# Optimization experiments

Hardware: AMD Instinct MI355X
Metric: run time of the kernel (lower is better)

The kernel has to match this reference:

```python
import jax, jax.numpy as jnp
import numpy as np

B, N, C = 2, 784, 384
D_STATE, D_CONV, EXPAND = 64, 4, 2
D_INNER = EXPAND * C           # 768
DT_RANK = -(-C // 16)          # 24
NB, BS = 4, C // 4             # EinFFT blocks
SCALE = 0.02


def setup_inputs() -> dict:
    key = jax.random.key(0)
    ks = jax.random.split(key, 16)
    rn = lambda k, s, sc=SCALE: jax.random.normal(k, s, jnp.float32) * sc
    A = jnp.tile(jnp.arange(1, D_STATE + 1, dtype=jnp.float32), (D_INNER, 1))
    return {
        'x': jax.random.normal(ks[0], (B, N, C), jnp.float32),
        'H': 28, 'W': 28,
        'ln1_w': jnp.ones((C,), jnp.float32), 'ln1_b': jnp.zeros((C,), jnp.float32),
        'in_proj_w': rn(ks[1], (2 * D_INNER, C)),
        'conv_w': rn(ks[2], (D_INNER, 1, D_CONV), 0.1),
        'conv_b': jnp.zeros((D_INNER,), jnp.float32),
        'x_proj_w': rn(ks[3], (DT_RANK + 2 * D_STATE, D_INNER)),
        'dt_proj_w': rn(ks[4], (D_INNER, DT_RANK), 0.1),
        'dt_proj_b': rn(ks[5], (D_INNER,), 0.1),
        'A_log': jnp.log(A),
        'Dp': jnp.ones((D_INNER,), jnp.float32),
        'out_proj_w': rn(ks[6], (C, D_INNER)),
        'ln2_w': jnp.ones((C,), jnp.float32), 'ln2_b': jnp.zeros((C,), jnp.float32),
        'cw1': rn(ks[7], (2, NB, BS, BS)), 'cb1': rn(ks[8], (2, NB, BS)),
        'cw2': rn(ks[9], (2, NB, BS, BS)), 'cb2': rn(ks[10], (2, NB, BS)),
    }


def _ln(x, w, b, eps=1e-5):
    mu = x.mean(-1, keepdims=True)
    var = ((x - mu) ** 2).mean(-1, keepdims=True)
    return (x - mu) * jax.lax.rsqrt(var + eps) * w + b


def _silu(x):
    return x * jax.nn.sigmoid(x)


def _mamba(x, in_proj_w, conv_w, conv_b, x_proj_w, dt_proj_w, dt_proj_b, A_log, Dp, out_proj_w):
    Bb, L, _ = x.shape
    di, ds = A_log.shape
    dt_rank = dt_proj_w.shape[1]
    xz = x @ in_proj_w.T                       # [B,L,2*di]
    xi, z = jnp.split(xz, 2, axis=-1)
    # causal depthwise conv1d (pad left d_conv-1)
    xc = jax.lax.conv_general_dilated(
        xi.transpose(0, 2, 1), conv_w, (1,), [(conv_w.shape[-1] - 1, 0)],
        feature_group_count=di, dimension_numbers=('NCH', 'OIH', 'NCH'))
    xc = _silu(xc + conv_b[None, :, None]).transpose(0, 2, 1)  # [B,L,di]
    dbl = xc @ x_proj_w.T
    dt, Bs, Cs = jnp.split(dbl, [dt_rank, dt_rank + ds], axis=-1)
    dt = jax.nn.softplus(dt @ dt_proj_w.T + dt_proj_b)          # [B,L,di]
    A = -jnp.exp(A_log)                                          # [di,ds]

    def step(h, inp):
        dt_t, B_t, C_t, u_t = inp                                # [B,di],[B,ds],[B,ds],[B,di]
        dA = jnp.exp(dt_t[:, :, None] * A)                       # [B,di,ds]
        h = h * dA + dt_t[:, :, None] * B_t[:, None, :] * u_t[:, :, None]
        y = jnp.einsum('bds,bs->bd', h, C_t)
        return h, y

    h0 = jnp.zeros((Bb, di, ds), x.dtype)
    xs = (dt.transpose(1, 0, 2), Bs.transpose(1, 0, 2), Cs.transpose(1, 0, 2), xc.transpose(1, 0, 2))
    _, ys = jax.lax.scan(step, h0, xs)                           # [L,B,di]
    y = ys.transpose(1, 0, 2) + xc * Dp
    y = y * _silu(z)
    return y @ out_proj_w.T


def _einfft(x, cw1, cb1, cw2, cb2, lam=0.01):
    Bb, Nn, Cc = x.shape
    nb, bs = cw1.shape[1], cw1.shape[2]
    xf = jnp.fft.fft2(x.reshape(Bb, Nn, nb, bs), axes=(1, 2), norm='ortho')
    mul = lambda t, w: jnp.einsum('...bd,bdk->...bk', t, w)
    r1 = jax.nn.relu(mul(xf.real, cw1[0]) - mul(xf.imag, cw1[1]) + cb1[0])
    i1 = jax.nn.relu(mul(xf.real, cw1[1]) + mul(xf.imag, cw1[0]) + cb1[1])
    r2 = mul(r1, cw2[0]) - mul(i1, cw2[1]) + cb2[0]
    i2 = mul(r1, cw2[1]) + mul(i1, cw2[0]) + cb2[1]
    shrink = lambda v: jnp.sign(v) * jnp.maximum(jnp.abs(v) - lam, 0.0)
    xcplx = shrink(r2) + 1j * shrink(i2)
    out = jnp.fft.ifft2(xcplx, axes=(1, 2), norm='ortho').real.astype(jnp.float32)
    return out.reshape(Bb, Nn, Cc)


def reference(x, H, W, ln1_w, ln1_b, in_proj_w, conv_w, conv_b, x_proj_w,
              dt_proj_w, dt_proj_b, A_log, Dp, out_proj_w, ln2_w, ln2_b,
              cw1, cb1, cw2, cb2):
    x = x + _mamba(_ln(x, ln1_w, ln1_b), in_proj_w, conv_w, conv_b, x_proj_w,
                   dt_proj_w, dt_proj_b, A_log, Dp, out_proj_w)
    x = x + _einfft(_ln(x, ln2_w, ln2_b), cw1, cb1, cw2, cb2)
    return x
```

## Files before the change

### kernel.cpp

```cpp
#include <hip/hip_runtime.h>
#include <math.h>

#define BB 2
#define NN 784
#define CC 384
#define DI 768
#define DS 64
#define DTR 24
#define ROWS (BB*NN)
#define NC 16
#define LC 49

typedef __attribute__((ext_vector_type(8))) short bf16x8;
typedef __attribute__((ext_vector_type(4))) float f32x4;

static __device__ inline short f2bf(float f){
  unsigned u = __float_as_uint(f);
  unsigned r = (u + 0x7fffu + ((u>>16)&1u)) >> 16;
  return (short)r;
}
static __device__ inline float bf2f(short v){
  return __uint_as_float(((unsigned)(unsigned short)v)<<16);
}
static __device__ inline float rdlane(float v, int t){
  return __uint_as_float(__builtin_amdgcn_readlane(__float_as_uint(v), t));
}
template<int CTRL>
static __device__ inline float qp_add(float x){
  int t = __builtin_amdgcn_update_dpp(0, __float_as_int(x), CTRL, 0xf, 0xf, false);
  return x + __int_as_float(t);
}
#define QP_XOR1 0xB1
#define QP_XOR2 0x4E

__global__ void k_zero4(float4* __restrict__ p, int n4){
  int i = blockIdx.x*256 + threadIdx.x;
  if (i < n4) p[i] = make_float4(0.f,0.f,0.f,0.f);
}

__global__ void k_ln(const float* __restrict__ x, const float* __restrict__ w,
                     const float* __restrict__ b, float* __restrict__ out, int rows){
  int row = blockIdx.x;
  if (row >= rows) return;
  int lane = threadIdx.x;
  const float* xr = x + (size_t)row*CC;
  float v[6]; float s = 0.f;
#pragma unroll
  for (int i=0;i<6;i++){ v[i] = xr[lane + 64*i]; s += v[i]; }
#pragma unroll
  for (int o=32;o;o>>=1) s += __shfl_xor(s,o);
  float mu = s * (1.f/CC);
  float vs = 0.f;
#pragma unroll
  for (int i=0;i<6;i++){ float d=v[i]-mu; vs += d*d; }
#pragma unroll
  for (int o=32;o;o>>=1) vs += __shfl_xor(vs,o);
  float rstd = rsqrtf(vs*(1.f/CC) + 1e-5f);
  float* orow = out + (size_t)row*CC;
#pragma unroll
  for (int i=0;i<6;i++){ int c = lane+64*i; orow[c] = (v[i]-mu)*rstd*w[c] + b[c]; }
}

__global__ void k_lnT(const float* __restrict__ x, const float* __restrict__ w,
                      const float* __restrict__ b, float* __restrict__ out){
  int row = blockIdx.x;
  if (row >= ROWS) return;
  int bb = row / NN, n = row % NN;
  int lane = threadIdx.x;
  const float* xr = x + (size_t)row*CC;
  float v[6]; float s = 0.f;
#pragma unroll
  for (int i=0;i<6;i++){ v[i] = xr[lane + 64*i]; s += v[i]; }
#pragma unroll
  for (int o=32;o;o>>=1) s += __shfl_xor(s,o);
  float mu = s * (1.f/CC);
  float vs = 0.f;
#pragma unroll
  for (int i=0;i<6;i++){ float d=v[i]-mu; vs += d*d; }
#pragma unroll
  for (int o=32;o;o>>=1) vs += __shfl_xor(vs,o);
  float rstd = rsqrtf(vs*(1.f/CC) + 1e-5f);
  float* ob = out + (size_t)bb*301056 + n;
#pragma unroll
  for (int i=0;i<6;i++){ int c = lane+64*i; ob[(size_t)c*NN] = (v[i]-mu)*rstd*w[c] + b[c]; }
}

template<int EPI, int ABF, int BBF, int SPLITK>
__global__ __launch_bounds__(256) void k_mgemm(
    const void* __restrict__ Ap, int lda, long long Azs,
    const void* __restrict__ Bp, int ldb, long long Bzs,
    const float* __restrict__ aux, int ldaux, long long auxzs,
    float* __restrict__ Y, int ldo, long long Ozs,
    int M, int N, int K, float alpha)
{
  __shared__ __align__(16) short As[64*32];
  __shared__ __align__(16) short Bs[64*32];
  int bz = blockIdx.z;
  int z  = bz / SPLITK, ks = bz % SPLITK;
  if (EPI == 1 || EPI == 2 || EPI == 3) aux += (size_t)z*auxzs;
  Y += (size_t)z*Ozs;
  int nk = (K + 31) >> 5;
  int per = (nk + SPLITK - 1) / SPLITK;
  int kbeg = ks*per*32;
  int kend = kbeg + per*32; if (kend > K) kend = K;
  int m0 = blockIdx.y*64, n0 = blockIdx.x*64;
  int t = threadIdx.x;
  int srow = t>>2, skg = t&3;
  int w = t>>6, lane = t&63;
  int wr = (w>>1)*32, wc = (w&1)*32;
  int l15 = lane&15, lh = lane>>4;
  f32x4 acc[2][2] = {};
  int sslot = skg ^ ((srow>>1)&3);
  for (int k0=kbeg; k0<kend; k0+=32){
    {
      int gm = m0 + srow, gk = k0 + skg*8;
      if (ABF){
        bf16x8 v = {};
        if (gm < M && gk < K) v = *(const bf16x8*)((const short*)Ap + (size_t)z*Azs + (size_t)gm*lda + gk);
        *(bf16x8*)(As + srow*32 + sslot*8) = v;
      } else {
        const float* Af = (const float*)Ap + (size_t)z*Azs;
        float4 v0 = {0,0,0,0}, v1 = {0,0,0,0};
        if (gm < M && gk < K){
          const float* p = Af + (size_t)gm*lda + gk;
          v0 = *(const float4*)p; v1 = *(const float4*)(p+4);
        }
        union { short s[8]; bf16x8 v; } pk;
        pk.s[0]=f2bf(v0.x); pk.s[1]=f2bf(v0.y); pk.s[2]=f2bf(v0.z); pk.s[3]=f2bf(v0.w);
        pk.s[4]=f2bf(v1.x); pk.s[5]=f2bf(v1.y); pk.s[6]=f2bf(v1.z); pk.s[7]=f2bf(v1.w);
        *(bf16x8*)(As + srow*32 + sslot*8) = pk.v;
      }
    }
    {
      int gn = n0 + srow, gk = k0 + skg*8;
      if (BBF){
        bf16x8 v = {};
        if (gn < N && gk < K) v = *(const bf16x8*)((const short*)Bp + (size_t)z*Bzs + (size_t)gn*ldb + gk);
        *(bf16x8*)(Bs + srow*32 + sslot*8) = v;
      } else {
        const float* Bf = (const float*)Bp + (size_t)z*Bzs;
        float4 v0 = {0,0,0,0}, v1 = {0,0,0,0};
        if (gn < N && gk < K){
          const float* p = Bf + (size_t)gn*ldb + gk;
          v0 = *(const float4*)p; v1 = *(const float4*)(p+4);
        }
        union { short s[8]; bf16x8 v; } pk;
        pk.s[0]=f2bf(v0.x); pk.s[1]=f2bf(v0.y); pk.s[2]=f2bf(v0.z); pk.s[3]=f2bf(v0.w);
        pk.s[4]=f2bf(v1.x); pk.s[5]=f2bf(v1.y); pk.s[6]=f2bf(v1.z); pk.s[7]=f2bf(v1.w);
        *(bf16x8*)(Bs + srow*32 + sslot*8) = pk.v;
      }
    }
    __syncthreads();
    bf16x8 af[2], bfr[2];
#pragma unroll
    for (int mi=0; mi<2; mi++){
      int row = wr + mi*16 + l15;
      af[mi] = *(const bf16x8*)(As + row*32 + ((lh ^ ((row>>1)&3))<<3));
    }
#pragma unroll
    for (int ni=0; ni<2; ni++){
      int col = wc + ni*16 + l15;
      bfr[ni] = *(const bf16x8*)(Bs + col*32 + ((lh ^ ((col>>1)&3))<<3));
    }
#pragma unroll
    for (int mi=0; mi<2; mi++)
#pragma unroll
      for (int ni=0; ni<2; ni++)
        acc[mi][ni] = __builtin_amdgcn_mfma_f32_16x16x32_bf16(af[mi], bfr[ni], acc[mi][ni], 0, 0, 0);
    __syncthreads();
  }
#pragma unroll
  for (int mi=0; mi<2; mi++){
#pragma unroll
    for (int ni=0; ni<2; ni++){
      int col = n0 + wc + ni*16 + l15;
      if (col >= N) continue;
#pragma unroll
      for (int j=0; j<4; j++){
        int row = m0 + wr + mi*16 + lh*4 + j;
        if (row >= M) continue;
        float v = acc[mi][ni][j];
        if (EPI == 0){ Y[(size_t)row*ldo + col] = v*alpha; }
        else if (EPI == 1){ Y[(size_t)row*ldo + col] = v*alpha + aux[(size_t)row*ldaux + col]; }
        else if (EPI == 2){ v += aux[col]; Y[(size_t)row*ldo + col] = fmaxf(v, 0.f); }
        else if (EPI == 3){ v += aux[col]; Y[(size_t)row*ldo + col] = copysignf(fmaxf(fabsf(v)-0.01f, 0.f), v); }
        else { atomicAdd(&Y[(size_t)row*ldo + col], v*alpha); }
      }
    }
  }
}

#define GBM 64
#define GBN 64
#define GBK 16
__global__ __launch_bounds__(256) void k_gemm(
    const float* __restrict__ X, int lda,
    const float* __restrict__ W,
    const float* __restrict__ bias,
    float* __restrict__ Y,
    int M, int N, int K)
{
  __shared__ float As[GBK][GBM+4];
  __shared__ float Bs[GBK][GBN+4];
  int m0 = blockIdx.y*GBM, n0 = blockIdx.x*GBN;
  int tid = threadIdx.x;
  int ty = tid>>4, tx = tid&15;
  float acc[4][4] = {{0.f}};
  for (int k0=0;k0<K;k0+=GBK){
#pragma unroll
    for (int l=0;l<4;l++){
      int e = tid + 256*l;
      int m = e>>4, kk = e&15;
      int gm = m0+m, gk = k0+kk;
      As[kk][m] = (gm<M && gk<K) ? X[(size_t)gm*lda+gk] : 0.f;
      int gn = n0+m;
      Bs[kk][m] = (gn<N && gk<K) ? W[(size_t)gn*K+gk] : 0.f;
    }
    __syncthreads();
#pragma unroll
    for (int kk=0;kk<GBK;kk++){
      float4 av = *(const float4*)&As[kk][ty*4];
      float4 bv = *(const float4*)&Bs[kk][tx*4];
      float a[4]={av.x,av.y,av.z,av.w}, b[4]={bv.x,bv.y,bv.z,bv.w};
#pragma unroll
      for (int i=0;i<4;i++)
#pragma unroll
        for (int j=0;j<4;j++) acc[i][j] += a[i]*b[j];
    }
    __syncthreads();
  }
#pragma unroll
  for (int i=0;i<4;i++){
    int gm = m0+ty*4+i; if (gm>=M) continue;
#pragma unroll
    for (int j=0;j<4;j++){
      int gn = n0+tx*4+j; if (gn>=N) continue;
      float v = acc[i][j] + bias[gn];
      v = (v>20.f)? v : log1pf(expf(v));
      Y[(size_t)gm*N+gn] = v;
    }
  }
}

__global__ void k_conv(const float* __restrict__ xz, const float* __restrict__ cw,
                       const float* __restrict__ cb, float* __restrict__ xc){
  int idx = blockIdx.x*256 + threadIdx.x;
  if (idx >= ROWS*DI) return;
  int d = idx % DI;
  int r = idx / DI;
  int b = r / NN, l = r % NN;
  float acc = cb[d];
#pragma unroll
  for (int t=0;t<4;t++){
    int ls = l-3+t;
    if (ls>=0) acc += cw[d*4+t] * xz[((size_t)(b*NN+ls))*1536 + d];
  }
  xc[(size_t)r*DI + d] = acc / (1.f + expf(-acc));
}

__global__ __launch_bounds__(256) void k_scan1(
    const float* __restrict__ dbl, const float* __restrict__ dtb,
    const float* __restrict__ xc, const float* __restrict__ A_log,
    short* __restrict__ hpart, float* __restrict__ sdt)
{
  __shared__ float Sb[LC*64];
  int gx = blockIdx.x;
  int bc = gx & 31, dgrp = gx >> 5;
  int b = bc >> 4, c = bc & 15;
  int wv = threadIdx.x >> 6, lane = threadIdx.x & 63;
  int d = dgrp*4 + wv;
  int t0 = c*LC;
  const float* dbr = dbl + ((size_t)(b*NN+t0))*152 + DTR;
  for (int i = threadIdx.x; i < LC*64; i += 256){
    int r = i >> 6, col = i & 63;
    Sb[i] = dbr[(size_t)r*152 + col];
  }
  __syncthreads();
  float A = -__expf(A_log[d*DS + lane]);
  const float* dtp = dtb + ((size_t)(b*NN+t0))*DI + d;
  const float* up  = xc  + ((size_t)(b*NN+t0))*DI + d;
  float dt0v = (lane<LC) ? dtp[(size_t)lane*DI] : 0.f;
  float u0v  = (lane<LC) ? up[(size_t)lane*DI]  : 0.f;
  float h = 0.f;
  for (int tb=0; tb<LC; tb+=7){
    float e[7], f[7];
#pragma unroll
    for (int j=0;j<7;j++){
      int t = tb+j;
      float dt = rdlane(dt0v, t);
      float u  = rdlane(u0v, t);
      e[j] = __expf(dt*A);
      f[j] = (dt*u)*Sb[t*64 + lane];
    }
#pragma unroll
    for (int j=0;j<7;j++) h = h*e[j] + f[j];
  }
  int bd = b*DI + d;
  hpart[((size_t)bd*NC + c)*DS + lane] = f2bf(h);
  float s = dt0v;
#pragma unroll
  for (int o=32;o;o>>=1) s += __shfl_xor(s,o);
  if (lane==0) sdt[bd*NC + c] = s;
}

__global__ __launch_bounds__(256) void k_scan2(
    const float* __restrict__ sdt, const float* __restrict__ A_log,
    short* __restrict__ hpart)
{
  int wid = (blockIdx.x*256 + threadIdx.x) >> 6;
  int lane = threadIdx.x & 63;
  if (wid >= BB*DI) return;
  int d = wid % DI;
  float A = -__expf(A_log[d*DS + lane]);
  short* hp = hpart + (size_t)wid*NC*DS + lane;
  const float* sp = sdt + wid*NC;
  float part[NC], pA[NC];
#pragma unroll
  for (int c=0;c<NC;c++){ part[c] = bf2f(hp[(size_t)c*DS]); pA[c] = __expf(A*sp[c]); }
  float h = 0.f;
#pragma unroll
  for (int c=0;c<NC;c++){
    hp[(size_t)c*DS] = f2bf(h);
    h = h*pA[c] + part[c];
  }
}

__global__ __launch_bounds__(256) void k_scan3(
    const float* __restrict__ dbl, const float* __restrict__ dtb,
    const float* __restrict__ xc, const float* __restrict__ xz,
    const float* __restrict__ A_log, const float* __restrict__ Dp,
    const short* __restrict__ hin, float* __restrict__ y)
{
  __shared__ float S[LC*128];
  __shared__ float red[4][LC*17];
  int gx = blockIdx.x;
  int bc = gx & 31, dgrp = gx >> 5;
  int b = bc >> 4, c = bc & 15;
  int wv = threadIdx.x >> 6, lane = threadIdx.x & 63;
  int d = dgrp*4 + wv;
  int t0 = c*LC;
  const float* dbr = dbl + ((size_t)(b*NN+t0))*152 + DTR;
  for (int i = threadIdx.x; i < LC*128; i += 256){
    int r = i >> 7, col = i & 127;
    int ln = col & 63, which = col >> 6;
    S[r*128 + ln*2 + which] = dbr[(size_t)r*152 + col];
  }
  __syncthreads();
  float A = -__expf(A_log[d*DS + lane]);
  float Dv = Dp[d];
  const float* dtp = dtb + ((size_t)(b*NN+t0))*DI + d;
  const float* up  = xc  + ((size_t)(b*NN+t0))*DI + d;
  const float* zp  = xz  + ((size_t)(b*NN+t0))*1536 + DI + d;
  float* yp = y + ((size_t)(b*NN+t0))*DI + d;
  float dt0v = (lane<LC) ? dtp[(size_t)lane*DI]  : 0.f;
  float u0v  = (lane<LC) ? up[(size_t)lane*DI]   : 0.f;
  float z0v  = (lane<LC) ? zp[(size_t)lane*1536] : 0.f;
  int bd = b*DI + d;
  float h = bf2f(hin[((size_t)bd*NC + c)*DS + lane]);
  float* rw = red[wv];
  int g = lane>>2;
  bool gl = (lane&3)==0;
  for (int tb=0; tb<LC; tb+=7){
    float e[7], f[7], Cv[7];
#pragma unroll
    for (int j=0;j<7;j++){
      int t = tb+j;
      float2 bcv = *(const float2*)&S[t*128 + lane*2];
      float dt = rdlane(dt0v, t);
      float u  = rdlane(u0v, t);
      e[j]  = __expf(dt*A);
      f[j]  = (dt*u)*bcv.x;
      Cv[j] = bcv.y;
    }
#pragma unroll
    for (int j=0;j<7;j++){
      h = h*e[j] + f[j];
      float p = h*Cv[j];
      p = qp_add<QP_XOR1>(p);
      p = qp_add<QP_XOR2>(p);
      if (gl) rw[(tb+j)*17 + g] = p;
    }
  }
  if (lane < LC){
    const float* rr = rw + lane*17;
    float a0 = rr[0]+rr[4]+rr[8] +rr[12];
    float a1 = rr[1]+rr[5]+rr[9] +rr[13];
    float a2 = rr[2]+rr[6]+rr[10]+rr[14];
    float a3 = rr[3]+rr[7]+rr[11]+rr[15];
    float yv = (a0+a1)+(a2+a3) + u0v*Dv;
    float z = z0v;
    yp[(size_t)lane*DI] = yv * (z/(1.f+__expf(-z)));
  }
}

__global__ void k_tw(short* __restrict__ Wcat, short* __restrict__ WT){
  int idx = blockIdx.x*256+threadIdx.x;
  if (idx >= 2*784*1568) return;
  if (idx < 784*1568){
    int n = idx / 1568, f = idx % 1568;
    int ff = (f<784)? f : f-784;
    int m = (int)(((long long)ff*(long long)n) % 784);
    float ang = 6.283185307179586f * (float)m / 784.f;
    float s, cval; sincosf(ang, &s, &cval);
    WT[(size_t)n*1568 + f] = f2bf((f<784)? cval : -s);
  } else {
    int r = idx - 784*1568;
    int f = r / 784, n = r % 784;
    int ff = (f<784)? f : f-784;
    int m = (int)(((long long)ff*(long long)n) % 784);
    float ang = 6.283185307179586f * (float)m / 784.f;
    float s, cval; sincosf(ang, &s, &cval);
    Wcat[(size_t)f*784 + n] = f2bf((f<784)? cval : -s);
  }
}

__global__ void k_prepw(const float* __restrict__ cw1, const float* __restrict__ cb1,
                        const float* __restrict__ cw2, const float* __restrict__ cb2,
                        short* __restrict__ W1, short* __restrict__ W2,
                        float* __restrict__ b1, float* __restrict__ b2){
  int idx = blockIdx.x*256+threadIdx.x;
  if (idx < 2*4*192*192){
    int l = idx / (4*192*192);
    int r = idx % (4*192*192);
    int d = r % 192; int j = (r/192) % 192; int bl = r/(192*192);
    int jj = j % 96, dd = d % 96;
    const float* cw = l ? cw2 : cw1;
    const float* w0 = cw + bl*9216;
    const float* w1 = cw + 4*9216 + bl*9216;
    float v;
    if (j < 96) v = (d < 96) ? w0[dd*96+jj] : -w1[dd*96+jj];
    else        v = (d < 96) ? w1[dd*96+jj] :  w0[dd*96+jj];
    (l ? W2 : W1)[r] = f2bf(v);
  }
  if (idx < 2*4*192){
    int l = idx / (4*192);
    int r = idx % (4*192);
    int j = r % 192; int bl = r/192;
    const float* cb = l ? cb2 : cb1;
    (l ? b2 : b1)[r] = (j<96) ? cb[bl*96 + j] : cb[384 + bl*96 + (j-96)];
  }
}

__global__ void k_cfft4(const float* __restrict__ Ybuf, float* __restrict__ tcat){
  int idx = blockIdx.x*256+threadIdx.x;
  if (idx >= BB*NN*96) return;
  int k = idx % 96; int r = idx / 96;
  int b = r / NN, f = r % NN;
  const float* fre = Ybuf + (size_t)b*602112 + (size_t)f*384;
  const float* fim = fre + 301056;
  float R0=fre[k], R1=fre[96+k], R2=fre[192+k], R3=fre[288+k];
  float I0=fim[k], I1=fim[96+k], I2=fim[192+k], I3=fim[288+k];
  float* tr = tcat + (size_t)r*768;
  tr[k]       = R0+R1+R2+R3;  tr[96+k]    = I0+I1+I2+I3;
  tr[192+k]   = R0+I1-R2-I3;  tr[192+96+k]= I0-R1-I2+R3;
  tr[384+k]   = R0-R1+R2-R3;  tr[384+96+k]= I0-I1+I2-I3;
  tr[576+k]   = R0-I1-R2+I3;  tr[576+96+k]= I0+R1-I2-R3;
}

__global__ void k_cifft4(const float* __restrict__ t2cat, float* __restrict__ YbufT){
  int idx = blockIdx.x*256+threadIdx.x;
  if (idx >= BB*NN*96) return;
  int f = idx % 784;
  int rest = idx / 784;
  int k = rest % 96;
  int b = rest / 96;
  const float* tr = t2cat + ((size_t)(b*NN+f))*768;
  float R0=tr[k],     I0=tr[96+k];
  float R1=tr[192+k], I1=tr[192+96+k];
  float R2=tr[384+k], I2=tr[384+96+k];
  float R3=tr[576+k], I3=tr[576+96+k];
  float* YT = YbufT + (size_t)b*602112;
  float gr[4], gi[4];
  gr[0]=R0+R1+R2+R3; gi[0]=I0+I1+I2+I3;
  gr[1]=R0-I1-R2+I3; gi[1]=I0+R1-I2-R3;
  gr[2]=R0-R1+R2-R3; gi[2]=I0-I1+I2-I3;
  gr[3]=R0+I1-R2-I3; gi[3]=I0-R1-I2+R3;
#pragma unroll
  for (int n=0;n<4;n++){
    int c = n*96 + k;
    YT[(size_t)c*1568 + f]       = gr[n];
    YT[(size_t)c*1568 + 784 + f] = gi[n];
  }
}

extern "C" void kernel_launch(void* const* d_in, const int* in_sizes, int n_in,
                              void* d_out, int out_size, void* d_ws, size_t ws_size,
                              hipStream_t stream){
  const float* x         = (const float*)d_in[0];
  const float* ln1_w     = (const float*)d_in[3];
  const float* ln1_b     = (const float*)d_in[4];
  const float* in_proj_w = (const float*)d_in[5];
  const float* conv_w    = (const float*)d_in[6];
  const float* conv_b    = (const float*)d_in[7];
  const float* x_proj_w  = (const float*)d_in[8];
  const float* dt_proj_w = (const float*)d_in[9];
  const float* dt_proj_b = (const float*)d_in[10];
  const float* A_log     = (const float*)d_in[11];
  const float* Dp        = (const float*)d_in[12];
  const float* out_proj_w= (const float*)d_in[13];
  const float* ln2_w     = (const float*)d_in[14];
  const float* ln2_b     = (const float*)d_in[15];
  const float* cw1       = (const float*)d_in[16];
  const float* cb1       = (const float*)d_in[17];
  const float* cw2       = (const float*)d_in[18];
  const float* cb2       = (const float*)d_in[19];

  float* ws = (float*)d_ws;
  float* ln   = ws;
  float* xz   = ws + 602112;
  float* xc   = ws + 3010560;
  float* dbl  = ws + 4214784;
  float* dtb  = ws + 4453120;
  float* yb   = ws + 5657344;
  float* x1   = ws + 6861568;
  short* hpart= (short*)(ws + 7463680);
  float* sdt  = ws + 8250112;
  short* Wcat = (short*)(ws + 602112);
  float* lnT  = ws + 1831424;
  float* Ybuf = ws + 2433536;
  short* WT   = (short*)(ws + 4453120);
  float* tcat = ws + 602112;
  float* o1cat= ws + 1806336;
  float* t2cat= ws + 3010560;
  float* YbufT= ws + 602112;
  short* W1c  = (short*)(ws + 7463680);
  short* W2c  = (short*)(ws + 7537408);
  float* b1c  = ws + 7611136;
  float* b2c  = ws + 7611904;

  k_ln<<<ROWS,64,0,stream>>>(x, ln1_w, ln1_b, ln, ROWS);
  k_mgemm<0,0,0,1><<<dim3(24,25,1),256,0,stream>>>(ln,384,0, in_proj_w,384,0, nullptr,0,0,
                                                   xz,1536,0, ROWS,1536,384, 1.f);
  k_conv<<<(ROWS*DI+255)/256,256,0,stream>>>(xz,conv_w,conv_b,xc);
  k_zero4<<<(238336/4+255)/256,256,0,stream>>>((float4*)dbl, 238336/4);
  k_mgemm<4,0,0,8><<<dim3(3,25,8),256,0,stream>>>(xc,768,0, x_proj_w,768,0, nullptr,0,0,
                                                  dbl,152,0, ROWS,152,768, 1.f);
  k_gemm<<<dim3(12,25),256,0,stream>>>(dbl,152,dt_proj_w,dt_proj_b,dtb,ROWS,768,24);
  k_scan1<<<32*192,256,0,stream>>>(dbl,dtb,xc,A_log,hpart,sdt);
  k_scan2<<<(BB*DI)/4,256,0,stream>>>(sdt,A_log,hpart);
  k_scan3<<<32*192,256,0,stream>>>(dbl,dtb,xc,xz,A_log,Dp,hpart,yb);
  hipMemcpyAsync(x1, x, (size_t)602112*4, hipMemcpyDeviceToDevice, stream);
  k_mgemm<4,0,0,4><<<dim3(6,25,4),256,0,stream>>>(yb,768,0, out_proj_w,768,0, nullptr,0,0,
                                                  x1,384,0, ROWS,384,768, 1.f);

  k_tw<<<(2*784*1568+255)/256,256,0,stream>>>(Wcat,WT);
  k_prepw<<<(2*4*192*192+255)/256,256,0,stream>>>(cw1,cb1,cw2,cb2,W1c,W2c,b1c,b2c);
  k_lnT<<<ROWS,64,0,stream>>>(x1, ln2_w, ln2_b, lnT);
  k_zero4<<<(1204224/4+255)/256,256,0,stream>>>((float4*)Ybuf, 1204224/4);
  k_mgemm<4,1,0,4><<<dim3(6,25,8),256,0,stream>>>(Wcat,784,0, lnT,784,301056, nullptr,0,0,
                                                  Ybuf,384,602112, 1568,384,784, 1.f/56.f);
  k_cfft4<<<(BB*NN*96+255)/256,256,0,stream>>>(Ybuf,tcat);
  k_mgemm<2,0,1,1><<<dim3(3,25,4),256,0,stream>>>(tcat,768,192, W1c,192,36864, b1c,0,192,
                                                  o1cat,768,192, ROWS,192,192, 1.f);
  k_mgemm<3,0,1,1><<<dim3(3,25,4),256,0,stream>>>(o1cat,768,192, W2c,192,36864, b2c,0,192,
                                                  t2cat,768,192, ROWS,192,192, 1.f);
  k_cifft4<<<(BB*NN*96+255)/256,256,0,stream>>>(t2cat,YbufT);
  hipMemcpyAsync(d_out, x1, (size_t)602112*4, hipMemcpyDeviceToDevice, stream);
  k_mgemm<4,1,0,7><<<dim3(6,13,14),256,0,stream>>>(WT,1568,0, YbufT,1568,602112, nullptr,0,0,
                                                   (float*)d_out,384,301056, 784,384,1568, 1.f/56.f);
}
```

Measured before the change: 257.4 us.

## Emit bf16 activations, register-prefetch GEMM tiles, exp2 in scans, merge prep kernels

LayerNorm, transposed LayerNorm and the 4-point FFT kernels now write bf16 instead of fp32, so the GEMMs that consume them read half the bytes and skip the in-kernel conversion. The tiled MFMA GEMM now loads the next K tile from global memory into registers while the current tile is computed, and exits early when a split-K slice is empty. The scan kernels use exp2 with A prescaled by log2(e) and precompute dt*u once per lane. The twiddle-table, weight-prep and Ybuf-zero kernels are merged into one launch, adding register pressure and bf16 rounding of more intermediates.

```diff
diff --git a/kernel.cpp b/kernel.cpp
--- a/kernel.cpp
+++ b/kernel.cpp
@@ -32,6 +32,7 @@
 }
 #define QP_XOR1 0xB1
 #define QP_XOR2 0x4E
+#define LOG2E 1.44269504088896f
 
 __global__ void k_zero4(float4* __restrict__ p, int n4){
   int i = blockIdx.x*256 + threadIdx.x;
@@ -39,7 +40,7 @@
 }
 
 __global__ void k_ln(const float* __restrict__ x, const float* __restrict__ w,
-                     const float* __restrict__ b, float* __restrict__ out, int rows){
+                     const float* __restrict__ b, short* __restrict__ out, int rows){
   int row = blockIdx.x;
   if (row >= rows) return;
   int lane = threadIdx.x;
@@ -56,13 +57,13 @@
 #pragma unroll
   for (int o=32;o;o>>=1) vs += __shfl_xor(vs,o);
   float rstd = rsqrtf(vs*(1.f/CC) + 1e-5f);
-  float* orow = out + (size_t)row*CC;
-#pragma unroll
-  for (int i=0;i<6;i++){ int c = lane+64*i; orow[c] = (v[i]-mu)*rstd*w[c] + b[c]; }
+  short* orow = out + (size_t)row*CC;
+#pragma unroll
+  for (int i=0;i<6;i++){ int c = lane+64*i; orow[c] = f2bf((v[i]-mu)*rstd*w[c] + b[c]); }
 }
 
 __global__ void k_lnT(const float* __restrict__ x, const float* __restrict__ w,
-                      const float* __restrict__ b, float* __restrict__ out){
+                      const float* __restrict__ b, short* __restrict__ out){
   int row = blockIdx.x;
   if (row >= ROWS) return;
   int bb = row / NN, n = row % NN;
@@ -80,9 +81,9 @@
 #pragma unroll
   for (int o=32;o;o>>=1) vs += __shfl_xor(vs,o);
   float rstd = rsqrtf(vs*(1.f/CC) + 1e-5f);
-  float* ob = out + (size_t)bb*301056 + n;
-#pragma unroll
-  for (int i=0;i<6;i++){ int c = lane+64*i; ob[(size_t)c*NN] = (v[i]-mu)*rstd*w[c] + b[c]; }
+  short* ob = out + (size_t)bb*301056 + n;
+#pragma unroll
+  for (int i=0;i<6;i++){ int c = lane+64*i; ob[(size_t)c*NN] = f2bf((v[i]-mu)*rstd*w[c] + b[c]); }
 }
 
 template<int EPI, int ABF, int BBF, int SPLITK>
@@ -103,6 +104,8 @@
   int per = (nk + SPLITK - 1) / SPLITK;
   int kbeg = ks*per*32;
   int kend = kbeg + per*32; if (kend > K) kend = K;
+  if (kend <= kbeg) return;
+  int ntile = (kend - kbeg + 31) >> 5;
   int m0 = blockIdx.y*64, n0 = blockIdx.x*64;
   int t = threadIdx.x;
   int srow = t>>2, skg = t&3;
@@ -111,46 +114,59 @@
   int l15 = lane&15, lh = lane>>4;
   f32x4 acc[2][2] = {};
   int sslot = skg ^ ((srow>>1)&3);
-  for (int k0=kbeg; k0<kend; k0+=32){
-    {
-      int gm = m0 + srow, gk = k0 + skg*8;
-      if (ABF){
-        bf16x8 v = {};
-        if (gm < M && gk < K) v = *(const bf16x8*)((const short*)Ap + (size_t)z*Azs + (size_t)gm*lda + gk);
-        *(bf16x8*)(As + srow*32 + sslot*8) = v;
-      } else {
-        const float* Af = (const float*)Ap + (size_t)z*Azs;
-        float4 v0 = {0,0,0,0}, v1 = {0,0,0,0};
-        if (gm < M && gk < K){
-          const float* p = Af + (size_t)gm*lda + gk;
-          v0 = *(const float4*)p; v1 = *(const float4*)(p+4);
-        }
-        union { short s[8]; bf16x8 v; } pk;
-        pk.s[0]=f2bf(v0.x); pk.s[1]=f2bf(v0.y); pk.s[2]=f2bf(v0.z); pk.s[3]=f2bf(v0.w);
-        pk.s[4]=f2bf(v1.x); pk.s[5]=f2bf(v1.y); pk.s[6]=f2bf(v1.z); pk.s[7]=f2bf(v1.w);
-        *(bf16x8*)(As + srow*32 + sslot*8) = pk.v;
+  int gmA = m0 + srow, gnB = n0 + srow;
+  int gko = skg*8;
+
+  bf16x8 vA = {}, vB = {};
+  float4 fA0, fA1, fB0, fB1;
+
+  auto LOAD = [&](int k0){
+    int gk = k0 + gko;
+    if (ABF){
+      bf16x8 v = {};
+      if (gmA < M && gk < K) v = *(const bf16x8*)((const short*)Ap + (size_t)z*Azs + (size_t)gmA*lda + gk);
+      vA = v;
+    } else {
+      fA0 = make_float4(0.f,0.f,0.f,0.f); fA1 = fA0;
+      if (gmA < M && gk < K){
+        const float* p = (const float*)Ap + (size_t)z*Azs + (size_t)gmA*lda + gk;
+        fA0 = *(const float4*)p; fA1 = *(const float4*)(p+4);
       }
     }
-    {
-      int gn = n0 + srow, gk = k0 + skg*8;
-      if (BBF){
-        bf16x8 v = {};
-        if (gn < N && gk < K) v = *(const bf16x8*)((const short*)Bp + (size_t)z*Bzs + (size_t)gn*ldb + gk);
-        *(bf16x8*)(Bs + srow*32 + sslot*8) = v;
-      } else {
-        const float* Bf = (const float*)Bp + (size_t)z*Bzs;
-        float4 v0 = {0,0,0,0}, v1 = {0,0,0,0};
-        if (gn < N && gk < K){
-          const float* p = Bf + (size_t)gn*ldb + gk;
-          v0 = *(const float4*)p; v1 = *(const float4*)(p+4);
-        }
-        union { short s[8]; bf16x8 v; } pk;
-        pk.s[0]=f2bf(v0.x); pk.s[1]=f2bf(v0.y); pk.s[2]=f2bf(v0.z); pk.s[3]=f2bf(v0.w);
-        pk.s[4]=f2bf(v1.x); pk.s[5]=f2bf(v1.y); pk.s[6]=f2bf(v1.z); pk.s[7]=f2bf(v1.w);
-        *(bf16x8*)(Bs + srow*32 + sslot*8) = pk.v;
+    if (BBF){
+      bf16x8 v = {};
+      if (gnB < N && gk < K) v = *(const bf16x8*)((const short*)Bp + (size_t)z*Bzs + (size_t)gnB*ldb + gk);
+      vB = v;
+    } else {
+      fB0 = make_float4(0.f,0.f,0.f,0.f); fB1 = fB0;
+      if (gnB < N && gk < K){
+        const float* p = (const float*)Bp + (size_t)z*Bzs + (size_t)gnB*ldb + gk;
+        fB0 = *(const float4*)p; fB1 = *(const float4*)(p+4);
       }
     }
+  };
+  auto STORE = [&](){
+    if (ABF) *(bf16x8*)(As + srow*32 + sslot*8) = vA;
+    else {
+      union { short s[8]; bf16x8 v; } pk;
+      pk.s[0]=f2bf(fA0.x); pk.s[1]=f2bf(fA0.y); pk.s[2]=f2bf(fA0.z); pk.s[3]=f2bf(fA0.w);
+      pk.s[4]=f2bf(fA1.x); pk.s[5]=f2bf(fA1.y); pk.s[6]=f2bf(fA1.z); pk.s[7]=f2bf(fA1.w);
+      *(bf16x8*)(As + srow*32 + sslot*8) = pk.v;
+    }
+    if (BBF) *(bf16x8*)(Bs + srow*32 + sslot*8) = vB;
+    else {
+      union { short s[8]; bf16x8 v; } pk;
+      pk.s[0]=f2bf(fB0.x); pk.s[1]=f2bf(fB0.y); pk.s[2]=f2bf(fB0.z); pk.s[3]=f2bf(fB0.w);
+      pk.s[4]=f2bf(fB1.x); pk.s[5]=f2bf(fB1.y); pk.s[6]=f2bf(fB1.z); pk.s[7]=f2bf(fB1.w);
+      *(bf16x8*)(Bs + srow*32 + sslot*8) = pk.v;
+    }
+  };
+
+  LOAD(kbeg);
+  for (int ti=0; ti<ntile; ++ti){
+    STORE();
     __syncthreads();
+    if (ti+1 < ntile) LOAD(kbeg + (ti+1)*32);
     bf16x8 af[2], bfr[2];
 #pragma unroll
     for (int mi=0; mi<2; mi++){
@@ -276,11 +292,12 @@
     Sb[i] = dbr[(size_t)r*152 + col];
   }
   __syncthreads();
-  float A = -__expf(A_log[d*DS + lane]);
+  float A2 = -__expf(A_log[d*DS + lane]) * LOG2E;
   const float* dtp = dtb + ((size_t)(b*NN+t0))*DI + d;
   const float* up  = xc  + ((size_t)(b*NN+t0))*DI + d;
   float dt0v = (lane<LC) ? dtp[(size_t)lane*DI] : 0.f;
   float u0v  = (lane<LC) ? up[(size_t)lane*DI]  : 0.f;
+  float du0v = dt0v * u0v;
   float h = 0.f;
   for (int tb=0; tb<LC; tb+=7){
     float e[7], f[7];
@@ -288,9 +305,9 @@
     for (int j=0;j<7;j++){
       int t = tb+j;
       float dt = rdlane(dt0v, t);
-      float u  = rdlane(u0v, t);
-      e[j] = __expf(dt*A);
-      f[j] = (dt*u)*Sb[t*64 + lane];
+      float du = rdlane(du0v, t);
+      e[j] = exp2f(dt*A2);
+      f[j] = du*Sb[t*64 + lane];
     }
 #pragma unroll
     for (int j=0;j<7;j++) h = h*e[j] + f[j];
@@ -346,7 +363,7 @@
     S[r*128 + ln*2 + which] = dbr[(size_t)r*152 + col];
   }
   __syncthreads();
-  float A = -__expf(A_log[d*DS + lane]);
+  float A2 = -__expf(A_log[d*DS + lane]) * LOG2E;
   float Dv = Dp[d];
   const float* dtp = dtb + ((size_t)(b*NN+t0))*DI + d;
   const float* up  = xc  + ((size_t)(b*NN+t0))*DI + d;
@@ -355,6 +372,7 @@
   float dt0v = (lane<LC) ? dtp[(size_t)lane*DI]  : 0.f;
   float u0v  = (lane<LC) ? up[(size_t)lane*DI]   : 0.f;
   float z0v  = (lane<LC) ? zp[(size_t)lane*1536] : 0.f;
+  float du0v = dt0v * u0v;
   int bd = b*DI + d;
   float h = bf2f(hin[((size_t)bd*NC + c)*DS + lane]);
   float* rw = red[wv];
@@ -367,9 +385,9 @@
       int t = tb+j;
       float2 bcv = *(const float2*)&S[t*128 + lane*2];
       float dt = rdlane(dt0v, t);
-      float u  = rdlane(u0v, t);
-      e[j]  = __expf(dt*A);
-      f[j]  = (dt*u)*bcv.x;
+      float du = rdlane(du0v, t);
+      e[j]  = exp2f(dt*A2);
+      f[j]  = du*bcv.x;
       Cv[j] = bcv.y;
     }
 #pragma unroll
@@ -393,9 +411,13 @@
   }
 }
 
-__global__ void k_tw(short* __restrict__ Wcat, short* __restrict__ WT){
+__global__ void k_prep(short* __restrict__ Wcat, short* __restrict__ WT,
+                       const float* __restrict__ cw1, const float* __restrict__ cb1,
+                       const float* __restrict__ cw2, const float* __restrict__ cb2,
+                       short* __restrict__ W1, short* __restrict__ W2,
+                       float* __restrict__ b1, float* __restrict__ b2,
+                       float4* __restrict__ Ybuf4){
   int idx = blockIdx.x*256+threadIdx.x;
-  if (idx >= 2*784*1568) return;
   if (idx < 784*1568){
     int n = idx / 1568, f = idx % 1568;
     int ff = (f<784)? f : f-784;
@@ -403,7 +425,7 @@
     float ang = 6.283185307179586f * (float)m / 784.f;
     float s, cval; sincosf(ang, &s, &cval);
     WT[(size_t)n*1568 + f] = f2bf((f<784)? cval : -s);
-  } else {
+  } else if (idx < 2*784*1568){
     int r = idx - 784*1568;
     int f = r / 784, n = r % 784;
     int ff = (f<784)? f : f-784;
@@ -412,13 +434,6 @@
     float s, cval; sincosf(ang, &s, &cval);
     Wcat[(size_t)f*784 + n] = f2bf((f<784)? cval : -s);
   }
-}
-
-__global__ void k_prepw(const float* __restrict__ cw1, const float* __restrict__ cb1,
-                        const float* __restrict__ cw2, const float* __restrict__ cb2,
-                        short* __restrict__ W1, short* __restrict__ W2,
-                        float* __restrict__ b1, float* __restrict__ b2){
-  int idx = blockIdx.x*256+threadIdx.x;
   if (idx < 2*4*192*192){
     int l = idx / (4*192*192);
     int r = idx % (4*192*192);
@@ -439,9 +454,10 @@
     const float* cb = l ? cb2 : cb1;
     (l ? b2 : b1)[r] = (j<96) ? cb[bl*96 + j] : cb[384 + bl*96 + (j-96)];
   }
-}
-
-__global__ void k_cfft4(const float* __restrict__ Ybuf, float* __restrict__ tcat){
+  if (idx < 301056) Ybuf4[idx] = make_float4(0.f,0.f,0.f,0.f);
+}
+
+__global__ void k_cfft4(const float* __restrict__ Ybuf, short* __restrict__ tcat){
   int idx = blockIdx.x*256+threadIdx.x;
   if (idx >= BB*NN*96) return;
   int k = idx % 96; int r = idx / 96;
@@ -450,11 +466,11 @@
   const float* fim = fre + 301056;
   float R0=fre[k], R1=fre[96+k], R2=fre[192+k], R3=fre[288+k];
   float I0=fim[k], I1=fim[96+k], I2=fim[192+k], I3=fim[288+k];
-  float* tr = tcat + (size_t)r*768;
-  tr[k]       = R0+R1+R2+R3;  tr[96+k]    = I0+I1+I2+I3;
-  tr[192+k]   = R0+I1-R2-I3;  tr[192+96+k]= I0-R1-I2+R3;
-  tr[384+k]   = R0-R1+R2-R3;  tr[384+96+k]= I0-I1+I2-I3;
-  tr[576+k]   = R0-I1-R2+I3;  tr[576+96+k]= I0+R1-I2-R3;
+  short* tr = tcat + (size_t)r*768;
+  tr[k]       = f2bf(R0+R1+R2+R3);  tr[96+k]    = f2bf(I0+I1+I2+I3);
+  tr[192+k]   = f2bf(R0+I1-R2-I3);  tr[192+96+k]= f2bf(I0-R1-I2+R3);
+  tr[384+k]   = f2bf(R0-R1+R2-R3);  tr[384+96+k]= f2bf(I0-I1+I2-I3);
+  tr[576+k]   = f2bf(R0-I1-R2+I3);  tr[576+96+k]= f2bf(I0+R1-I2-R3);
 }
 
 __global__ void k_cifft4(const float* __restrict__ t2cat, float* __restrict__ YbufT){
@@ -506,7 +522,7 @@
   const float* cb2       = (const float*)d_in[19];
 
   float* ws = (float*)d_ws;
-  float* ln   = ws;
+  short* lnb  = (short*)ws;
   float* xz   = ws + 602112;
   float* xc   = ws + 3010560;
   float* dbl  = ws + 4214784;
@@ -516,10 +532,10 @@
   short* hpart= (short*)(ws + 7463680);
   float* sdt  = ws + 8250112;
   short* Wcat = (short*)(ws + 602112);
-  float* lnT  = ws + 1831424;
+  short* lnT  = (short*)(ws + 1831424);
   float* Ybuf = ws + 2433536;
   short* WT   = (short*)(ws + 4453120);
-  float* tcat = ws + 602112;
+  short* tcat = (short*)(ws + 602112);
   float* o1cat= ws + 1806336;
   float* t2cat= ws + 3010560;
   float* YbufT= ws + 602112;
@@ -528,8 +544,8 @@
   float* b1c  = ws + 7611136;
   float* b2c  = ws + 7611904;
 
-  k_ln<<<ROWS,64,0,stream>>>(x, ln1_w, ln1_b, ln, ROWS);
-  k_mgemm<0,0,0,1><<<dim3(24,25,1),256,0,stream>>>(ln,384,0, in_proj_w,384,0, nullptr,0,0,
+  k_ln<<<ROWS,64,0,stream>>>(x, ln1_w, ln1_b, lnb, ROWS);
+  k_mgemm<0,1,0,1><<<dim3(24,25,1),256,0,stream>>>(lnb,384,0, in_proj_w,384,0, nullptr,0,0,
                                                    xz,1536,0, ROWS,1536,384, 1.f);
   k_conv<<<(ROWS*DI+255)/256,256,0,stream>>>(xz,conv_w,conv_b,xc);
   k_zero4<<<(238336/4+255)/256,256,0,stream>>>((float4*)dbl, 238336/4);
@@ -543,14 +559,12 @@
   k_mgemm<4,0,0,4><<<dim3(6,25,4),256,0,stream>>>(yb,768,0, out_proj_w,768,0, nullptr,0,0,
                                                   x1,384,0, ROWS,384,768, 1.f);
 
-  k_tw<<<(2*784*1568+255)/256,256,0,stream>>>(Wcat,WT);
-  k_prepw<<<(2*4*192*192+255)/256,256,0,stream>>>(cw1,cb1,cw2,cb2,W1c,W2c,b1c,b2c);
+  k_prep<<<(2*784*1568+255)/256,256,0,stream>>>(Wcat,WT,cw1,cb1,cw2,cb2,W1c,W2c,b1c,b2c,(float4*)Ybuf);
   k_lnT<<<ROWS,64,0,stream>>>(x1, ln2_w, ln2_b, lnT);
-  k_zero4<<<(1204224/4+255)/256,256,0,stream>>>((float4*)Ybuf, 1204224/4);
-  k_mgemm<4,1,0,4><<<dim3(6,25,8),256,0,stream>>>(Wcat,784,0, lnT,784,301056, nullptr,0,0,
+  k_mgemm<4,1,1,4><<<dim3(6,25,8),256,0,stream>>>(Wcat,784,0, lnT,784,301056, nullptr,0,0,
                                                   Ybuf,384,602112, 1568,384,784, 1.f/56.f);
   k_cfft4<<<(BB*NN*96+255)/256,256,0,stream>>>(Ybuf,tcat);
-  k_mgemm<2,0,1,1><<<dim3(3,25,4),256,0,stream>>>(tcat,768,192, W1c,192,36864, b1c,0,192,
+  k_mgemm<2,1,1,1><<<dim3(3,25,4),256,0,stream>>>(tcat,768,192, W1c,192,36864, b1c,0,192,
                                                   o1cat,768,192, ROWS,192,192, 1.f);
   k_mgemm<3,0,1,1><<<dim3(3,25,4),256,0,stream>>>(o1cat,768,192, W2c,192,36864, b2c,0,192,
                                                   t2cat,768,192, ROWS,192,192, 1.f);
```

Result: faster. 249.4 us (-3.1%).
